# Performance work log

Hardware: AMD Instinct MI355X
Metric: run time of the kernel (lower is better)

## Reference

```python
import jax, jax.numpy as jnp
import numpy as np

DIM = 1024
D_STATE = 64
D_CONV = 4
EXPAND = 2
HEADDIM = 64
D_INNER = EXPAND * DIM                      # 2048
NHEADS = D_INNER // HEADDIM                 # 32
D_CONV_DIM = D_INNER + 2 * D_STATE          # 2176 (ngroups=1)
D_IN_PROJ = 2 * D_INNER + 2 * D_STATE + NHEADS  # 4256


def setup_inputs() -> dict:
    key = jax.random.key(0)
    ks = jax.random.split(key, 9)
    B, L = 4, 2048
    x = jax.random.normal(ks[0], (B, L, DIM), dtype=jnp.float32)
    in_proj_w = jax.random.normal(ks[1], (D_IN_PROJ, DIM), dtype=jnp.float32) * 0.02
    conv_w = jax.random.normal(ks[2], (D_CONV_DIM, D_CONV), dtype=jnp.float32) * 0.2
    conv_b = jax.random.normal(ks[3], (D_CONV_DIM,), dtype=jnp.float32) * 0.02
    # dt bias from inverse-softplus of dt ~ U(1e-3, 0.1) (mamba2 init)
    dt = jnp.exp(jax.random.uniform(ks[4], (NHEADS,)) * (np.log(0.1) - np.log(1e-3)) + np.log(1e-3))
    dt_bias = (dt + jnp.log(-jnp.expm1(-dt))).astype(jnp.float32)
    A_log = jnp.log(jax.random.uniform(ks[5], (NHEADS,), minval=1.0, maxval=16.0)).astype(jnp.float32)
    D = jnp.ones((NHEADS,), dtype=jnp.float32)
    norm_w = jnp.ones((D_INNER,), dtype=jnp.float32)
    out_proj_w = jax.random.normal(ks[6], (DIM, D_INNER), dtype=jnp.float32) * 0.02
    return {"x": x, "in_proj_w": in_proj_w, "conv_w": conv_w, "conv_b": conv_b,
            "dt_bias": dt_bias, "A_log": A_log, "D": D, "norm_w": norm_w,
            "out_proj_w": out_proj_w}


def _mamba2_fwd(x, in_proj_w, conv_w, conv_b, dt_bias, A_log, D, norm_w, out_proj_w):
    B, L, _ = x.shape
    zxbcdt = jnp.einsum('bld,ed->ble', x, in_proj_w)  # (B,L,4256)
    z = zxbcdt[..., :D_INNER]
    xBC = zxbcdt[..., D_INNER:D_INNER + D_CONV_DIM]
    dt = jax.nn.softplus(zxbcdt[..., D_INNER + D_CONV_DIM:] + dt_bias)  # (B,L,H)
    # causal depthwise conv (kernel D_CONV) + silu
    xp = jnp.pad(xBC, ((0, 0), (D_CONV - 1, 0), (0, 0)))
    conv = conv_b
    for k in range(D_CONV):
        conv = conv + xp[:, k:k + L, :] * conv_w[:, k]
    xBC = jax.nn.silu(conv)
    x_ssm = xBC[..., :D_INNER].reshape(B, L, NHEADS, HEADDIM)
    Bm = xBC[..., D_INNER:D_INNER + D_STATE]          # (B,L,N) ngroups=1
    Cm = xBC[..., D_INNER + D_STATE:]                 # (B,L,N)
    A = -jnp.exp(A_log)                               # (H,)

    def step(h, inp):
        xt, Bt, Ct, dtt = inp                         # (B,H,P),(B,N),(B,N),(B,H)
        dA = jnp.exp(dtt * A)                         # (B,H)
        h = h * dA[:, :, None, None] + (dtt[:, :, None] * xt)[..., None] * Bt[:, None, None, :]
        y = jnp.einsum('bhpn,bn->bhp', h, Ct)
        return h, y

    h0 = jnp.zeros((B, NHEADS, HEADDIM, D_STATE), dtype=x.dtype)
    xs = (jnp.swapaxes(x_ssm, 0, 1), jnp.swapaxes(Bm, 0, 1),
          jnp.swapaxes(Cm, 0, 1), jnp.swapaxes(dt, 0, 1))
    _, ys = jax.lax.scan(step, h0, xs)                # (L,B,H,P)
    y = jnp.swapaxes(ys, 0, 1) + x_ssm * D[None, None, :, None]
    y = y.reshape(B, L, D_INNER)
    # gated RMSNorm (norm_before_gate=False): norm(y * silu(z))
    g = y * jax.nn.silu(z)
    g = g * jax.lax.rsqrt(jnp.mean(g * g, axis=-1, keepdims=True) + 1e-5) * norm_w
    return jnp.einsum('ble,de->bld', g, out_proj_w)


def reference(x, in_proj_w, conv_w, conv_b, dt_bias, A_log, D, norm_w, out_proj_w):
    return _mamba2_fwd(x, in_proj_w, conv_w, conv_b, dt_bias, A_log, D, norm_w, out_proj_w)
```

## Files before the change

kernel.cpp:

```cpp
#include <hip/hip_runtime.h>
#include <stdint.h>

typedef unsigned short ushort_t;
typedef __attribute__((ext_vector_type(4))) float f32x4;
typedef __attribute__((ext_vector_type(8))) short short8;
typedef __attribute__((ext_vector_type(4))) unsigned short us4;

#define L_SEQ   2048
#define NROWS   8192
#define KDIM    1024
#define DINNER  2048
#define NHEADS  32
#define DSTATE  64
#define DCONVD  2176
#define NPROJ   4256
#define NPROJP  4352
#define LDZX    4352
#define NCHUNK  32

__device__ __forceinline__ float bf2f(ushort_t u) {
    union { uint32_t i; float f; } v; v.i = ((uint32_t)u) << 16; return v.f;
}
__device__ __forceinline__ ushort_t f2bf(float f) {
    uint32_t x = __float_as_uint(f);
    x += 0x7FFFu + ((x >> 16) & 1u);
    return (ushort_t)(x >> 16);
}
__device__ __forceinline__ int swzi(int row, int col) {
    return row * 64 + (col ^ ((row & 7) << 3));
}

__global__ __launch_bounds__(256) void cast_bf16_kernel(const float* __restrict__ in,
                                                        ushort_t* __restrict__ out, int n4) {
    int i = blockIdx.x * 256 + threadIdx.x;
    if (i >= n4) return;
    float4 v = ((const float4*)in)[i];
    ushort4 o;
    o.x = f2bf(v.x); o.y = f2bf(v.y); o.z = f2bf(v.z); o.w = f2bf(v.w);
    ((ushort4*)out)[i] = o;
}

__global__ __launch_bounds__(256) void cast_pad_w_kernel(const float* __restrict__ w,
                                                         ushort_t* __restrict__ out) {
    int i = blockIdx.x * 256 + threadIdx.x;
    int idx = i * 4;
    int row = idx >> 10;
    ushort4 o;
    if (row < NPROJ) {
        float4 v = ((const float4*)w)[i];
        o.x = f2bf(v.x); o.y = f2bf(v.y); o.z = f2bf(v.z); o.w = f2bf(v.w);
    } else {
        o.x = 0; o.y = 0; o.z = 0; o.w = 0;
    }
    ((ushort4*)out)[i] = o;
}

__device__ __forceinline__ void async16(const void* g, void* l) {
    __builtin_amdgcn_global_load_lds((const __attribute__((address_space(1))) void*)g,
                                     (__attribute__((address_space(3))) void*)l, 16, 0, 0);
}

template<int BN, bool OUT_BF16>
__global__ __launch_bounds__(512, 1) void gemm256_kernel(const ushort_t* __restrict__ Ap,
                                                         const ushort_t* __restrict__ Bp,
                                                         void* __restrict__ Cp,
                                                         const int K, const int ldc,
                                                         const int ntn) {
    constexpr int NBH = BN / 128;
    constexpr int FC  = BN / 64;
    __shared__ ushort_t ldsA[2][2][8192];
    __shared__ ushort_t ldsB[2][NBH][8192];

    const int tid = threadIdx.x;
    const int w = tid >> 6, l = tid & 63;
    const int lr = l & 15, lk = l >> 4;
    const int wm = w >> 2, wn = w & 3;

    const int lin = blockIdx.x;
    const int cpx = gridDim.x >> 3;
    const int swz = (lin & 7) * cpx + (lin >> 3);
    const int nt = swz % ntn, mt = swz / ntn;
    const int m0 = mt * 256, n0 = nt * BN;

    const int row0 = tid >> 3,          c0 = (tid & 7) ^ (row0 & 7);
    const int row1 = (512 + tid) >> 3,  c1 = ((512 + tid) & 7) ^ (row1 & 7);

    const int bcol = wn * (BN / 4);
    const int bh = bcol >> 7, bw0 = bcol & 127;

    f32x4 acc[8][FC];
    const f32x4 zero = {0.f, 0.f, 0.f, 0.f};
#pragma unroll
    for (int i = 0; i < 8; ++i)
#pragma unroll
        for (int j = 0; j < FC; ++j) acc[i][j] = zero;

    auto stage = [&](int d_, int isB, int h_, int ktn) {
        const ushort_t* gb = (isB ? Bp + (size_t)(n0 + h_ * 128) * K
                                  : Ap + (size_t)(m0 + h_ * 128) * K) + (size_t)ktn * 64;
        ushort_t* lb = isB ? &ldsB[d_][h_][0] : &ldsA[d_][h_][0];
        async16(gb + (size_t)row0 * K + c0 * 8, lb + w * 512);
        async16(gb + (size_t)row1 * K + c1 * 8, lb + 4096 + w * 512);
    };

#define COMPUTE_KS(ks_) do {                                                          \
        short8 af[8], bfv[FC];                                                        \
        _Pragma("unroll")                                                             \
        for (int fr = 0; fr < 8; ++fr) {                                              \
            const int ar = fr * 16 + lr;                                              \
            af[fr] = *(const short8*)&Ah[ar * 64 + ((((ks_) * 4 + lk) ^ (ar & 7)) << 3)]; \
        }                                                                             \
        _Pragma("unroll")                                                             \
        for (int fc = 0; fc < FC; ++fc) {                                             \
            const int br = bw0 + fc * 16 + lr;                                        \
            bfv[fc] = *(const short8*)&Bh[br * 64 + ((((ks_) * 4 + lk) ^ (br & 7)) << 3)]; \
        }                                                                             \
        __builtin_amdgcn_s_setprio(1);                                                \
        _Pragma("unroll")                                                             \
        for (int fr = 0; fr < 8; ++fr)                                                \
            _Pragma("unroll")                                                         \
            for (int fc = 0; fc < FC; ++fc)                                           \
                acc[fr][fc] = __builtin_amdgcn_mfma_f32_16x16x32_bf16(                \
                    af[fr], bfv[fc], acc[fr][fc], 0, 0, 0);                           \
        __builtin_amdgcn_s_setprio(0);                                                \
    } while (0)

    stage(0, 0, 0, 0); stage(0, 1, 0, 0);
    stage(0, 0, 1, 0);
    if (NBH == 2) stage(0, 1, 1, 0);

    const int NKT = K >> 6;
    for (int kt = 0; kt < NKT; ++kt) {
        const int d = kt & 1;
        const bool more = (kt + 1 < NKT);
        const ushort_t* Ah = &ldsA[d][wm][0];
        const ushort_t* Bh = &ldsB[d][bh][0];

        if (more) { stage(d ^ 1, 0, 0, kt + 1); stage(d ^ 1, 1, 0, kt + 1); }
        if (more) asm volatile("s_waitcnt vmcnt(4)" ::: "memory");
        else      asm volatile("s_waitcnt vmcnt(0)" ::: "memory");
        __builtin_amdgcn_s_barrier();

        COMPUTE_KS(0);

        if (more) { stage(d ^ 1, 0, 1, kt + 1); if (NBH == 2) stage(d ^ 1, 1, 1, kt + 1); }

        COMPUTE_KS(1);

        __builtin_amdgcn_s_barrier();
    }
#undef COMPUTE_KS

#pragma unroll
    for (int fr2 = 0; fr2 < 8; ++fr2)
#pragma unroll
        for (int fc2 = 0; fc2 < FC; ++fc2) {
            const int col = n0 + bcol + fc2 * 16 + lr;
            const int rowb = m0 + wm * 128 + fr2 * 16 + lk * 4;
#pragma unroll
            for (int r = 0; r < 4; ++r) {
                if (OUT_BF16)
                    ((ushort_t*)Cp)[(size_t)(rowb + r) * ldc + col] = f2bf(acc[fr2][fc2][r]);
                else
                    ((float*)Cp)[(size_t)(rowb + r) * ldc + col] = acc[fr2][fc2][r];
            }
        }
}

__global__ __launch_bounds__(256) void conv_silu_kernel(const ushort_t* __restrict__ zx,
                                                        const float* __restrict__ conv_w,
                                                        const float* __restrict__ conv_b,
                                                        ushort_t* __restrict__ convout) {
    const int idx = blockIdx.x * 256 + threadIdx.x;
    const int row = idx / 272;
    const int c = (idx - row * 272) * 8;
    const int l = row & (L_SEQ - 1);
    float acc[8];
    {
        const float4* bp = (const float4*)(conv_b + c);
        float4 b0 = bp[0], b1 = bp[1];
        acc[0] = b0.x; acc[1] = b0.y; acc[2] = b0.z; acc[3] = b0.w;
        acc[4] = b1.x; acc[5] = b1.y; acc[6] = b1.z; acc[7] = b1.w;
    }
    float wv[8][4];
    {
        const float4* wp = (const float4*)(conv_w + c * 4);
#pragma unroll
        for (int i = 0; i < 8; ++i) {
            float4 t = wp[i];
            wv[i][0] = t.x; wv[i][1] = t.y; wv[i][2] = t.z; wv[i][3] = t.w;
        }
    }
#pragma unroll
    for (int k = 0; k < 4; ++k) {
        const int ll = l - 3 + k;
        if (ll >= 0) {
            short8 v = *(const short8*)(zx + (size_t)(row - 3 + k) * LDZX + DINNER + c);
#pragma unroll
            for (int i = 0; i < 8; ++i)
                acc[i] += bf2f((ushort_t)v[i]) * wv[i][k];
        }
    }
    short8 o;
#pragma unroll
    for (int i = 0; i < 8; ++i) {
        float s = acc[i] / (1.f + expf(-acc[i]));
        o[i] = (short)f2bf(s);
    }
    *(short8*)(convout + (size_t)row * DCONVD + c) = o;
}

__global__ __launch_bounds__(256) void dt_kernel(const ushort_t* __restrict__ zx,
                                                 const float* __restrict__ dt_bias,
                                                 float* __restrict__ dtb) {
    int idx = blockIdx.x * 256 + threadIdx.x;
    int row = idx >> 5;
    int h = idx & 31;
    float v = bf2f(zx[(size_t)row * LDZX + NPROJ - NHEADS + h]) + dt_bias[h];
    dtb[idx] = (v > 20.f) ? v : log1pf(expf(v));
}

__global__ __launch_bounds__(256) void chunk_intra_kernel(
    const ushort_t* __restrict__ cvb, const float* __restrict__ dtb,
    const float* __restrict__ A_log, const float* __restrict__ Dvec,
    ushort_t* __restrict__ ybuf, ushort_t* __restrict__ Gbuf,
    float* __restrict__ expPb)
{
    const int c = blockIdx.x, h = blockIdx.y, b = blockIdx.z;
    const int tid = threadIdx.x;
    const int wv = tid >> 6, lane = tid & 63;
    const int lr = lane & 15, lk = lane >> 4;

    __shared__ __align__(16) ushort_t Cs[4096];
    __shared__ __align__(16) ushort_t Bs[4096];
    __shared__ __align__(16) ushort_t Xt[4096];
    __shared__ __align__(16) ushort_t Ss[4096];
    __shared__ __align__(16) ushort_t Bw[4096];
    __shared__ float sP[64], sdt[64], sWf[64];

    const int t4 = tid >> 2, qq = tid & 3;
    const size_t rowg0 = (size_t)b * L_SEQ + c * 64;
    const ushort_t* rowp = cvb + (rowg0 + t4) * DCONVD;

    short8 rb0 = *(const short8*)(rowp + DINNER + qq * 16);
    short8 rb1 = *(const short8*)(rowp + DINNER + qq * 16 + 8);
    short8 rc0 = *(const short8*)(rowp + DINNER + DSTATE + qq * 16);
    short8 rc1 = *(const short8*)(rowp + DINNER + DSTATE + qq * 16 + 8);
    short8 rx0 = *(const short8*)(rowp + h * 64 + qq * 16);
    short8 rx1 = *(const short8*)(rowp + h * 64 + qq * 16 + 8);

    *(short8*)&Cs[swzi(t4, qq * 16)]     = rc0;
    *(short8*)&Cs[swzi(t4, qq * 16 + 8)] = rc1;
    *(short8*)&Bs[swzi(t4, qq * 16)]     = rb0;
    *(short8*)&Bs[swzi(t4, qq * 16 + 8)] = rb1;
#pragma unroll
    for (int k = 0; k < 8; ++k) {
        Xt[swzi(qq * 16 + k, t4)]     = (ushort_t)rx0[k];
        Xt[swzi(qq * 16 + 8 + k, t4)] = (ushort_t)rx1[k];
    }
    if (tid < 64) {
        float dt = dtb[(rowg0 + tid) * NHEADS + h];
        float A = -__expf(A_log[h]);
        float P = dt * A;
#pragma unroll
        for (int off = 1; off < 64; off <<= 1) {
            float o = __shfl_up(P, off);
            if (tid >= off) P += o;
        }
        sP[tid] = P;
        sdt[tid] = dt;
        float P63 = __shfl(P, 63);
        sWf[tid] = __expf(P63 - P) * dt;
        expPb[(size_t)(b * NHEADS + h) * L_SEQ + c * 64 + tid] = __expf(P);
    }
    __syncthreads();

    {
        const float w = sWf[t4];
#pragma unroll
        for (int k = 0; k < 8; ++k) {
            Bw[swzi(qq * 16 + k, t4)]     = f2bf(bf2f((ushort_t)rb0[k]) * w);
            Bw[swzi(qq * 16 + 8 + k, t4)] = f2bf(bf2f((ushort_t)rb1[k]) * w);
        }
    }

    const float Dh = Dvec[h];
    {
        short8 a0 = *(const short8*)&Cs[swzi(wv * 16 + lr, lk * 8)];
        short8 a1 = *(const short8*)&Cs[swzi(wv * 16 + lr, 32 + lk * 8)];
        f32x4 acc[4];
        const f32x4 zero = {0.f, 0.f, 0.f, 0.f};
#pragma unroll
        for (int nj = 0; nj < 4; ++nj) {
            short8 b0 = *(const short8*)&Bs[swzi(nj * 16 + lr, lk * 8)];
            short8 b1 = *(const short8*)&Bs[swzi(nj * 16 + lr, 32 + lk * 8)];
            acc[nj] = __builtin_amdgcn_mfma_f32_16x16x32_bf16(a0, b0, zero, 0, 0, 0);
            acc[nj] = __builtin_amdgcn_mfma_f32_16x16x32_bf16(a1, b1, acc[nj], 0, 0, 0);
        }
#pragma unroll
        for (int r = 0; r < 4; ++r) {
            const int i = wv * 16 + lk * 4 + r;
            const float Pi = sP[i];
#pragma unroll
            for (int nj = 0; nj < 4; ++nj) {
                const int j = nj * 16 + lr;
                float s = 0.f;
                if (j <= i) s = acc[nj][r] * __expf(Pi - sP[j]) * sdt[j];
                if (j == i) s += Dh;
                Ss[swzi(i, j)] = f2bf(s);
            }
        }
    }
    __syncthreads();

    {
        short8 a0 = *(const short8*)&Ss[swzi(wv * 16 + lr, lk * 8)];
        short8 a1 = *(const short8*)&Ss[swzi(wv * 16 + lr, 32 + lk * 8)];
        const f32x4 zero = {0.f, 0.f, 0.f, 0.f};
#pragma unroll
        for (int np = 0; np < 4; ++np) {
            short8 b0 = *(const short8*)&Xt[swzi(np * 16 + lr, lk * 8)];
            short8 b1 = *(const short8*)&Xt[swzi(np * 16 + lr, 32 + lk * 8)];
            f32x4 acc = __builtin_amdgcn_mfma_f32_16x16x32_bf16(a0, b0, zero, 0, 0, 0);
            acc = __builtin_amdgcn_mfma_f32_16x16x32_bf16(a1, b1, acc, 0, 0, 0);
#pragma unroll
            for (int r = 0; r < 4; ++r) {
                const int i = wv * 16 + lk * 4 + r;
                const int p = np * 16 + lr;
                ybuf[(rowg0 + i) * DINNER + (size_t)h * 64 + p] = f2bf(acc[r]);
            }
        }
    }

    {
        short8 a0 = *(const short8*)&Xt[swzi(wv * 16 + lr, lk * 8)];
        short8 a1 = *(const short8*)&Xt[swzi(wv * 16 + lr, 32 + lk * 8)];
        const f32x4 zero = {0.f, 0.f, 0.f, 0.f};
        const size_t gbase = ((size_t)((b * NHEADS + h) * NCHUNK + c)) << 12;
#pragma unroll
        for (int nt = 0; nt < 4; ++nt) {
            short8 b0 = *(const short8*)&Bw[swzi(nt * 16 + lr, lk * 8)];
            short8 b1 = *(const short8*)&Bw[swzi(nt * 16 + lr, 32 + lk * 8)];
            f32x4 acc = __builtin_amdgcn_mfma_f32_16x16x32_bf16(a0, b0, zero, 0, 0, 0);
            acc = __builtin_amdgcn_mfma_f32_16x16x32_bf16(a1, b1, acc, 0, 0, 0);
#pragma unroll
            for (int r = 0; r < 4; ++r) {
                const int p = wv * 16 + lk * 4 + r;
                const int n = nt * 16 + lr;
                Gbuf[gbase + p * 64 + n] = f2bf(acc[r]);
            }
        }
    }
}

__global__ __launch_bounds__(256) void state_scan_kernel(
    ushort_t* __restrict__ GH, const float* __restrict__ expPb)
{
    const int half = blockIdx.x, h = blockIdx.y, b = blockIdx.z;
    const int bh = b * NHEADS + h;
    const int e0 = half * 2048 + threadIdx.x * 8;
    ushort_t* base = GH + ((size_t)bh << 17);
    const float* ep = expPb + (size_t)bh * L_SEQ;

    float hr[8];
#pragma unroll
    for (int k = 0; k < 8; ++k) hr[k] = 0.f;

    short8 g = *(const short8*)(base + e0);
    float Ec = ep[63];
    for (int c = 0; c < NCHUNK; ++c) {
        short8 gn = g; float En = 0.f;
        if (c + 1 < NCHUNK) {
            gn = *(const short8*)(base + ((size_t)(c + 1) << 12) + e0);
            En = ep[(c + 1) * 64 + 63];
        }
        short8 o;
#pragma unroll
        for (int k = 0; k < 8; ++k) o[k] = (short)f2bf(hr[k]);
        *(short8*)(base + ((size_t)c << 12) + e0) = o;
#pragma unroll
        for (int k = 0; k < 8; ++k) hr[k] = hr[k] * Ec + bf2f((ushort_t)g[k]);
        g = gn; Ec = En;
    }
}

__global__ __launch_bounds__(256) void y_inter_kernel(
    const ushort_t* __restrict__ cvb, const float* __restrict__ expPb,
    const ushort_t* __restrict__ hst, ushort_t* __restrict__ ybuf)
{
    const int c = blockIdx.x + 1, h = blockIdx.y, b = blockIdx.z;
    const int tid = threadIdx.x;
    const int wv = tid >> 6, lane = tid & 63;
    const int lr = lane & 15, lk = lane >> 4;
    const int bh = b * NHEADS + h;

    __shared__ __align__(16) ushort_t Cs[4096];
    __shared__ __align__(16) ushort_t Hp[4096];
    __shared__ float sEp[64];

    const int t4 = tid >> 2, qq = tid & 3;
    const size_t rowg0 = (size_t)b * L_SEQ + c * 64;
    {
        const ushort_t* rp = cvb + (rowg0 + t4) * DCONVD + DINNER + DSTATE + qq * 16;
        *(short8*)&Cs[swzi(t4, qq * 16)]     = *(const short8*)rp;
        *(short8*)&Cs[swzi(t4, qq * 16 + 8)] = *(const short8*)(rp + 8);
        const ushort_t* hr = hst + (((size_t)(bh * NCHUNK + c)) << 12) + t4 * 64 + qq * 16;
        *(short8*)&Hp[swzi(t4, qq * 16)]     = *(const short8*)hr;
        *(short8*)&Hp[swzi(t4, qq * 16 + 8)] = *(const short8*)(hr + 8);
    }
    if (tid < 64) sEp[tid] = expPb[(size_t)bh * L_SEQ + c * 64 + tid];
    __syncthreads();

    short8 a0 = *(const short8*)&Cs[swzi(wv * 16 + lr, lk * 8)];
    short8 a1 = *(const short8*)&Cs[swzi(wv * 16 + lr, 32 + lk * 8)];
    const f32x4 zero = {0.f, 0.f, 0.f, 0.f};
#pragma unroll
    for (int np = 0; np < 4; ++np) {
        short8 b0 = *(const short8*)&Hp[swzi(np * 16 + lr, lk * 8)];
        short8 b1 = *(const short8*)&Hp[swzi(np * 16 + lr, 32 + lk * 8)];
        f32x4 acc = __builtin_amdgcn_mfma_f32_16x16x32_bf16(a0, b0, zero, 0, 0, 0);
        acc = __builtin_amdgcn_mfma_f32_16x16x32_bf16(a1, b1, acc, 0, 0, 0);
#pragma unroll
        for (int r = 0; r < 4; ++r) {
            const int t = wv * 16 + lk * 4 + r;
            const int p = np * 16 + lr;
            ushort_t* yp = &ybuf[(rowg0 + t) * DINNER + (size_t)h * 64 + p];
            *yp = f2bf(bf2f(*yp) + acc[r] * sEp[t]);
        }
    }
}

__global__ __launch_bounds__(256) void gatenorm_kernel(const ushort_t* __restrict__ ybuf,
                                                       const ushort_t* __restrict__ zx,
                                                       const float* __restrict__ norm_w,
                                                       ushort_t* __restrict__ gbuf) {
    const int row = blockIdx.x;
    const int tid = threadIdx.x;
    short8 yv = *(const short8*)(ybuf + (size_t)row * DINNER + tid * 8);
    short8 zv = *(const short8*)(zx + (size_t)row * LDZX + tid * 8);
    float g[8];
    float ss = 0.f;
#pragma unroll
    for (int i = 0; i < 8; ++i) {
        float y = bf2f((ushort_t)yv[i]);
        float z = bf2f((ushort_t)zv[i]);
        float sz = z / (1.f + expf(-z));
        float gg = y * sz;
        g[i] = gg;
        ss += gg * gg;
    }
#pragma unroll
    for (int o = 32; o > 0; o >>= 1) ss += __shfl_xor(ss, o);
    __shared__ float wsum[4];
    if ((tid & 63) == 0) wsum[tid >> 6] = ss;
    __syncthreads();
    float tot = wsum[0] + wsum[1] + wsum[2] + wsum[3];
    float scale = rsqrtf(tot * (1.0f / (float)DINNER) + 1e-5f);
    short8 o8;
#pragma unroll
    for (int i = 0; i < 8; ++i)
        o8[i] = (short)f2bf(g[i] * scale * norm_w[tid * 8 + i]);
    *(short8*)(gbuf + (size_t)row * DINNER + tid * 8) = o8;
}

extern "C" void kernel_launch(void* const* d_in, const int* in_sizes, int n_in,
                              void* d_out, int out_size, void* d_ws, size_t ws_size,
                              hipStream_t stream) {
    const float* x          = (const float*)d_in[0];
    const float* in_proj_w  = (const float*)d_in[1];
    const float* conv_w     = (const float*)d_in[2];
    const float* conv_b     = (const float*)d_in[3];
    const float* dt_bias    = (const float*)d_in[4];
    const float* A_log      = (const float*)d_in[5];
    const float* Dvec       = (const float*)d_in[6];
    const float* norm_w     = (const float*)d_in[7];
    const float* out_proj_w = (const float*)d_in[8];
    float* out = (float*)d_out;

    char* ws = (char*)d_ws;
    size_t off = 0;
    ushort_t* owbf  = (ushort_t*)(ws + off); off += (size_t)KDIM * DINNER * 2;
    ushort_t* zx    = (ushort_t*)(ws + off); off += (size_t)NROWS * LDZX * 2;
    ushort_t* cvb   = (ushort_t*)(ws + off); off += (size_t)NROWS * DCONVD * 2;
    float*    dtb   = (float*)(ws + off);    off += (size_t)NROWS * NHEADS * 4;
    float*    expPb = (float*)(ws + off);    off += (size_t)128 * L_SEQ * 4;
    ushort_t* ybuf  = (ushort_t*)(ws + off); off += (size_t)NROWS * DINNER * 2;
    char* tail = ws + off;
    ushort_t* xbf  = (ushort_t*)tail;
    ushort_t* wbf  = (ushort_t*)(tail + (size_t)NROWS * KDIM * 2);
    ushort_t* Gbuf = (ushort_t*)tail;
    ushort_t* gbuf = (ushort_t*)tail;

    cast_bf16_kernel<<<8192, 256, 0, stream>>>(x, xbf, NROWS * KDIM / 4);
    cast_pad_w_kernel<<<4352, 256, 0, stream>>>(in_proj_w, wbf);
    cast_bf16_kernel<<<2048, 256, 0, stream>>>(out_proj_w, owbf, KDIM * DINNER / 4);

    gemm256_kernel<256, true><<<544, 512, 0, stream>>>(xbf, wbf, zx, KDIM, LDZX, 17);

    conv_silu_kernel<<<NROWS * 272 / 256, 256, 0, stream>>>(zx, conv_w, conv_b, cvb);

    dt_kernel<<<NROWS * NHEADS / 256, 256, 0, stream>>>(zx, dt_bias, dtb);

    chunk_intra_kernel<<<dim3(NCHUNK, NHEADS, 4), 256, 0, stream>>>(
        cvb, dtb, A_log, Dvec, ybuf, Gbuf, expPb);
    state_scan_kernel<<<dim3(2, NHEADS, 4), 256, 0, stream>>>(Gbuf, expPb);
    y_inter_kernel<<<dim3(NCHUNK - 1, NHEADS, 4), 256, 0, stream>>>(
        cvb, expPb, Gbuf, ybuf);

    gatenorm_kernel<<<NROWS, 256, 0, stream>>>(ybuf, zx, norm_w, gbuf);

    gemm256_kernel<128, false><<<256, 512, 0, stream>>>(gbuf, owbf, out, DINNER, KDIM, 8);
}
```

Measured before the change: 329.2 us.

## Restructure GEMM main loop into four-phase k-half pipeline and fuse dt softplus

```diff
diff --git a/kernel.cpp b/kernel.cpp
--- a/kernel.cpp
+++ b/kernel.cpp
@@ -66,10 +66,11 @@
                                                          void* __restrict__ Cp,
                                                          const int K, const int ldc,
                                                          const int ntn) {
-    constexpr int NBH = BN / 128;
-    constexpr int FC  = BN / 64;
-    __shared__ ushort_t ldsA[2][2][8192];
-    __shared__ ushort_t ldsB[2][NBH][8192];
+    constexpr int FC = BN / 64;
+    constexpr int LB = BN / 128;
+    constexpr int VN = 2 + LB;
+    __shared__ ushort_t ldsA[2][2][256 * 32];
+    __shared__ ushort_t ldsB[2][2][BN * 32];
 
     const int tid = threadIdx.x;
     const int w = tid >> 6, l = tid & 63;
@@ -81,12 +82,10 @@
     const int swz = (lin & 7) * cpx + (lin >> 3);
     const int nt = swz % ntn, mt = swz / ntn;
     const int m0 = mt * 256, n0 = nt * BN;
-
-    const int row0 = tid >> 3,          c0 = (tid & 7) ^ (row0 & 7);
-    const int row1 = (512 + tid) >> 3,  c1 = ((512 + tid) & 7) ^ (row1 & 7);
-
     const int bcol = wn * (BN / 4);
-    const int bh = bcol >> 7, bw0 = bcol & 127;
+
+    const int sr0 = tid >> 2,         sg0 = (tid & 3) ^ (sr0 & 3) ^ ((sr0 >> 2) & 3);
+    const int sr1 = (512 + tid) >> 2, sg1 = ((512 + tid) & 3) ^ (sr1 & 3) ^ ((sr1 >> 2) & 3);
 
     f32x4 acc[8][FC];
     const f32x4 zero = {0.f, 0.f, 0.f, 0.f};
@@ -95,61 +94,73 @@
 #pragma unroll
         for (int j = 0; j < FC; ++j) acc[i][j] = zero;
 
-    auto stage = [&](int d_, int isB, int h_, int ktn) {
-        const ushort_t* gb = (isB ? Bp + (size_t)(n0 + h_ * 128) * K
-                                  : Ap + (size_t)(m0 + h_ * 128) * K) + (size_t)ktn * 64;
-        ushort_t* lb = isB ? &ldsB[d_][h_][0] : &ldsA[d_][h_][0];
-        async16(gb + (size_t)row0 * K + c0 * 8, lb + w * 512);
-        async16(gb + (size_t)row1 * K + c1 * 8, lb + 4096 + w * 512);
+    auto stageA = [&](int d_, int kh, int ktn) {
+        const ushort_t* gb = Ap + (size_t)m0 * K + (size_t)ktn * 64 + kh * 32;
+        async16(gb + (size_t)sr0 * K + sg0 * 8, (ushort_t*)&ldsA[d_][kh][0] + tid * 8);
+        async16(gb + (size_t)sr1 * K + sg1 * 8, (ushort_t*)&ldsA[d_][kh][0] + (512 + tid) * 8);
     };
-
-#define COMPUTE_KS(ks_) do {                                                          \
-        short8 af[8], bfv[FC];                                                        \
-        _Pragma("unroll")                                                             \
-        for (int fr = 0; fr < 8; ++fr) {                                              \
-            const int ar = fr * 16 + lr;                                              \
-            af[fr] = *(const short8*)&Ah[ar * 64 + ((((ks_) * 4 + lk) ^ (ar & 7)) << 3)]; \
-        }                                                                             \
-        _Pragma("unroll")                                                             \
-        for (int fc = 0; fc < FC; ++fc) {                                             \
-            const int br = bw0 + fc * 16 + lr;                                        \
-            bfv[fc] = *(const short8*)&Bh[br * 64 + ((((ks_) * 4 + lk) ^ (br & 7)) << 3)]; \
-        }                                                                             \
-        __builtin_amdgcn_s_setprio(1);                                                \
-        _Pragma("unroll")                                                             \
-        for (int fr = 0; fr < 8; ++fr)                                                \
-            _Pragma("unroll")                                                         \
-            for (int fc = 0; fc < FC; ++fc)                                           \
-                acc[fr][fc] = __builtin_amdgcn_mfma_f32_16x16x32_bf16(                \
-                    af[fr], bfv[fc], acc[fr][fc], 0, 0, 0);                           \
-        __builtin_amdgcn_s_setprio(0);                                                \
+    auto stageB = [&](int d_, int kh, int ktn) {
+        const ushort_t* gb = Bp + (size_t)n0 * K + (size_t)ktn * 64 + kh * 32;
+        async16(gb + (size_t)sr0 * K + sg0 * 8, (ushort_t*)&ldsB[d_][kh][0] + tid * 8);
+        if constexpr (LB == 2)
+            async16(gb + (size_t)sr1 * K + sg1 * 8, (ushort_t*)&ldsB[d_][kh][0] + (512 + tid) * 8);
+    };
+
+#define VMWAIT_VN do { if constexpr (VN == 4) asm volatile("s_waitcnt vmcnt(4)" ::: "memory"); \
+                       else                   asm volatile("s_waitcnt vmcnt(3)" ::: "memory"); } while (0)
+#define VMWAIT_0  asm volatile("s_waitcnt vmcnt(0)" ::: "memory")
+
+    short8 bfv[FC];
+
+#define PHASE(ks_, frh_, STAGE_STMT, VM_STMT) do {                                      \
+        short8 af[4];                                                                   \
+        _Pragma("unroll")                                                               \
+        for (int fr = 0; fr < 4; ++fr) {                                                \
+            const int row = wm * 128 + ((frh_) * 4 + fr) * 16 + lr;                     \
+            const int sl = lk ^ (row & 3) ^ ((row >> 2) & 3);                           \
+            af[fr] = *(const short8*)&ldsA[d][ks_][row * 32 + sl * 8];                  \
+        }                                                                               \
+        if ((frh_) == 0) {                                                              \
+            _Pragma("unroll")                                                           \
+            for (int fc = 0; fc < FC; ++fc) {                                           \
+                const int row = bcol + fc * 16 + lr;                                    \
+                const int sl = lk ^ (row & 3) ^ ((row >> 2) & 3);                       \
+                bfv[fc] = *(const short8*)&ldsB[d][ks_][row * 32 + sl * 8];             \
+            }                                                                           \
+        }                                                                               \
+        STAGE_STMT;                                                                     \
+        __builtin_amdgcn_s_barrier();                                                   \
+        __builtin_amdgcn_s_setprio(1);                                                  \
+        _Pragma("unroll")                                                               \
+        for (int fr = 0; fr < 4; ++fr)                                                  \
+            _Pragma("unroll")                                                           \
+            for (int fc = 0; fc < FC; ++fc)                                             \
+                acc[(frh_) * 4 + fr][fc] = __builtin_amdgcn_mfma_f32_16x16x32_bf16(     \
+                    af[fr], bfv[fc], acc[(frh_) * 4 + fr][fc], 0, 0, 0);                \
+        __builtin_amdgcn_s_setprio(0);                                                  \
+        VM_STMT;                                                                        \
+        __builtin_amdgcn_s_barrier();                                                   \
     } while (0)
 
-    stage(0, 0, 0, 0); stage(0, 1, 0, 0);
-    stage(0, 0, 1, 0);
-    if (NBH == 2) stage(0, 1, 1, 0);
+    stageA(0, 0, 0); stageB(0, 0, 0);
+    stageA(0, 1, 0); stageB(0, 1, 0);
+    VMWAIT_VN;
+    __builtin_amdgcn_s_barrier();
 
     const int NKT = K >> 6;
     for (int kt = 0; kt < NKT; ++kt) {
         const int d = kt & 1;
         const bool more = (kt + 1 < NKT);
-        const ushort_t* Ah = &ldsA[d][wm][0];
-        const ushort_t* Bh = &ldsB[d][bh][0];
-
-        if (more) { stage(d ^ 1, 0, 0, kt + 1); stage(d ^ 1, 1, 0, kt + 1); }
-        if (more) asm volatile("s_waitcnt vmcnt(4)" ::: "memory");
-        else      asm volatile("s_waitcnt vmcnt(0)" ::: "memory");
-        __builtin_amdgcn_s_barrier();
-
-        COMPUTE_KS(0);
-
-        if (more) { stage(d ^ 1, 0, 1, kt + 1); if (NBH == 2) stage(d ^ 1, 1, 1, kt + 1); }
-
-        COMPUTE_KS(1);
-
-        __builtin_amdgcn_s_barrier();
-    }
-#undef COMPUTE_KS
+        PHASE(0, 0, { if (more) stageA(d ^ 1, 0, kt + 1); }, {});
+        PHASE(0, 1, { if (more) stageB(d ^ 1, 0, kt + 1); },
+                    { if (more) VMWAIT_VN; else VMWAIT_0; });
+        PHASE(1, 0, { if (more) stageA(d ^ 1, 1, kt + 1); }, {});
+        PHASE(1, 1, { if (more) stageB(d ^ 1, 1, kt + 1); },
+                    { if (more) VMWAIT_VN; });
+    }
+#undef PHASE
+#undef VMWAIT_VN
+#undef VMWAIT_0
 
 #pragma unroll
     for (int fr2 = 0; fr2 < 8; ++fr2)
@@ -210,18 +221,9 @@
     *(short8*)(convout + (size_t)row * DCONVD + c) = o;
 }
 
-__global__ __launch_bounds__(256) void dt_kernel(const ushort_t* __restrict__ zx,
-                                                 const float* __restrict__ dt_bias,
-                                                 float* __restrict__ dtb) {
-    int idx = blockIdx.x * 256 + threadIdx.x;
-    int row = idx >> 5;
-    int h = idx & 31;
-    float v = bf2f(zx[(size_t)row * LDZX + NPROJ - NHEADS + h]) + dt_bias[h];
-    dtb[idx] = (v > 20.f) ? v : log1pf(expf(v));
-}
-
 __global__ __launch_bounds__(256) void chunk_intra_kernel(
-    const ushort_t* __restrict__ cvb, const float* __restrict__ dtb,
+    const ushort_t* __restrict__ cvb, const ushort_t* __restrict__ zx,
+    const float* __restrict__ dt_bias,
     const float* __restrict__ A_log, const float* __restrict__ Dvec,
     ushort_t* __restrict__ ybuf, ushort_t* __restrict__ Gbuf,
     float* __restrict__ expPb)
@@ -259,7 +261,8 @@
         Xt[swzi(qq * 16 + 8 + k, t4)] = (ushort_t)rx1[k];
     }
     if (tid < 64) {
-        float dt = dtb[(rowg0 + tid) * NHEADS + h];
+        float dv = bf2f(zx[(rowg0 + tid) * LDZX + (NPROJ - NHEADS) + h]) + dt_bias[h];
+        float dt = (dv > 20.f) ? dv : log1pf(expf(dv));
         float A = -__expf(A_log[h]);
         float P = dt * A;
 #pragma unroll
@@ -482,7 +485,6 @@
     ushort_t* owbf  = (ushort_t*)(ws + off); off += (size_t)KDIM * DINNER * 2;
     ushort_t* zx    = (ushort_t*)(ws + off); off += (size_t)NROWS * LDZX * 2;
     ushort_t* cvb   = (ushort_t*)(ws + off); off += (size_t)NROWS * DCONVD * 2;
-    float*    dtb   = (float*)(ws + off);    off += (size_t)NROWS * NHEADS * 4;
     float*    expPb = (float*)(ws + off);    off += (size_t)128 * L_SEQ * 4;
     ushort_t* ybuf  = (ushort_t*)(ws + off); off += (size_t)NROWS * DINNER * 2;
     char* tail = ws + off;
@@ -499,10 +501,8 @@
 
     conv_silu_kernel<<<NROWS * 272 / 256, 256, 0, stream>>>(zx, conv_w, conv_b, cvb);
 
-    dt_kernel<<<NROWS * NHEADS / 256, 256, 0, stream>>>(zx, dt_bias, dtb);
-
     chunk_intra_kernel<<<dim3(NCHUNK, NHEADS, 4), 256, 0, stream>>>(
-        cvb, dtb, A_log, Dvec, ybuf, Gbuf, expPb);
+        cvb, zx, dt_bias, A_log, Dvec, ybuf, Gbuf, expPb);
     state_scan_kernel<<<dim3(2, NHEADS, 4), 256, 0, stream>>>(Gbuf, expPb);
     y_inter_kernel<<<dim3(NCHUNK - 1, NHEADS, 4), 256, 0, stream>>>(
         cvb, expPb, Gbuf, ybuf);
```

Result: no change. 325.7 us (-1.1%).

## Fuse conv+silu and softplus dt into chunk kernel, use 128-tile in_proj GEMM

Applied to the files above, without the earlier changes.

```diff
diff --git a/kernel.cpp b/kernel.cpp
--- a/kernel.cpp
+++ b/kernel.cpp
@@ -58,6 +58,102 @@
 __device__ __forceinline__ void async16(const void* g, void* l) {
     __builtin_amdgcn_global_load_lds((const __attribute__((address_space(1))) void*)g,
                                      (__attribute__((address_space(3))) void*)l, 16, 0, 0);
+}
+
+__global__ __launch_bounds__(256, 2) void gemm128_kernel(const ushort_t* __restrict__ Ap,
+                                                         const ushort_t* __restrict__ Bp,
+                                                         ushort_t* __restrict__ Cx) {
+    __shared__ ushort_t ldsA[2][8192];
+    __shared__ ushort_t ldsB[2][8192];
+    const int tid = threadIdx.x;
+    const int w = tid >> 6, l = tid & 63;
+    const int lr = l & 15, lk = l >> 4;
+    const int wm = w >> 1, wn = w & 1;
+
+    const int lin = blockIdx.x;
+    const int swz = (lin & 7) * 272 + (lin >> 3);
+    const int nt = swz % 34, mt = swz / 34;
+    const int m0 = mt * 128, n0 = nt * 128;
+
+    int srow[4], scol[4];
+#pragma unroll
+    for (int i = 0; i < 4; ++i) {
+        int s = i * 256 + tid;
+        srow[i] = s >> 3;
+        scol[i] = (s & 7) ^ (srow[i] & 7);
+    }
+
+    f32x4 acc[4][4];
+    const f32x4 zero = {0.f, 0.f, 0.f, 0.f};
+#pragma unroll
+    for (int i = 0; i < 4; ++i)
+#pragma unroll
+        for (int j = 0; j < 4; ++j) acc[i][j] = zero;
+
+    auto stageA = [&](int d_, int ktn) {
+        const ushort_t* gb = Ap + (size_t)m0 * KDIM + (size_t)ktn * 64;
+#pragma unroll
+        for (int i = 0; i < 4; ++i)
+            async16(gb + (size_t)srow[i] * KDIM + scol[i] * 8, &ldsA[d_][(i * 256 + tid) * 8]);
+    };
+    auto stageB = [&](int d_, int ktn) {
+        const ushort_t* gb = Bp + (size_t)n0 * KDIM + (size_t)ktn * 64;
+#pragma unroll
+        for (int i = 0; i < 4; ++i)
+            async16(gb + (size_t)srow[i] * KDIM + scol[i] * 8, &ldsB[d_][(i * 256 + tid) * 8]);
+    };
+
+#define CKS(ks_) do {                                                                   \
+        short8 af[4], bfv[4];                                                           \
+        _Pragma("unroll")                                                               \
+        for (int fr = 0; fr < 4; ++fr) {                                                \
+            const int ar = wm * 64 + fr * 16 + lr;                                      \
+            af[fr] = *(const short8*)&ldsA[d][ar * 64 + ((((ks_) * 4 + lk) ^ (ar & 7)) << 3)]; \
+        }                                                                               \
+        _Pragma("unroll")                                                               \
+        for (int fc = 0; fc < 4; ++fc) {                                                \
+            const int br = wn * 64 + fc * 16 + lr;                                      \
+            bfv[fc] = *(const short8*)&ldsB[d][br * 64 + ((((ks_) * 4 + lk) ^ (br & 7)) << 3)]; \
+        }                                                                               \
+        __builtin_amdgcn_s_setprio(1);                                                  \
+        _Pragma("unroll")                                                               \
+        for (int fr = 0; fr < 4; ++fr)                                                  \
+            _Pragma("unroll")                                                           \
+            for (int fc = 0; fc < 4; ++fc)                                              \
+                acc[fr][fc] = __builtin_amdgcn_mfma_f32_16x16x32_bf16(                  \
+                    af[fr], bfv[fc], acc[fr][fc], 0, 0, 0);                             \
+        __builtin_amdgcn_s_setprio(0);                                                  \
+    } while (0)
+
+    stageA(0, 0); stageB(0, 0);
+    asm volatile("s_waitcnt vmcnt(0)" ::: "memory");
+    __builtin_amdgcn_s_barrier();
+
+    const int NKT = KDIM >> 6;
+    for (int kt = 0; kt < NKT; ++kt) {
+        const int d = kt & 1;
+        const bool more = (kt + 1 < NKT);
+        if (more) stageA(d ^ 1, kt + 1);
+        if (more) asm volatile("s_waitcnt vmcnt(4)" ::: "memory");
+        else      asm volatile("s_waitcnt vmcnt(0)" ::: "memory");
+        __builtin_amdgcn_s_barrier();
+        CKS(0);
+        if (more) stageB(d ^ 1, kt + 1);
+        CKS(1);
+        __builtin_amdgcn_s_barrier();
+    }
+#undef CKS
+
+#pragma unroll
+    for (int fr2 = 0; fr2 < 4; ++fr2)
+#pragma unroll
+        for (int fc2 = 0; fc2 < 4; ++fc2) {
+            const int col = n0 + wn * 64 + fc2 * 16 + lr;
+            const int rowb = m0 + wm * 64 + fr2 * 16 + lk * 4;
+#pragma unroll
+            for (int r = 0; r < 4; ++r)
+                Cx[(size_t)(rowb + r) * LDZX + col] = f2bf(acc[fr2][fc2][r]);
+        }
 }
 
 template<int BN, bool OUT_BF16>
@@ -167,64 +263,12 @@
         }
 }
 
-__global__ __launch_bounds__(256) void conv_silu_kernel(const ushort_t* __restrict__ zx,
-                                                        const float* __restrict__ conv_w,
-                                                        const float* __restrict__ conv_b,
-                                                        ushort_t* __restrict__ convout) {
-    const int idx = blockIdx.x * 256 + threadIdx.x;
-    const int row = idx / 272;
-    const int c = (idx - row * 272) * 8;
-    const int l = row & (L_SEQ - 1);
-    float acc[8];
-    {
-        const float4* bp = (const float4*)(conv_b + c);
-        float4 b0 = bp[0], b1 = bp[1];
-        acc[0] = b0.x; acc[1] = b0.y; acc[2] = b0.z; acc[3] = b0.w;
-        acc[4] = b1.x; acc[5] = b1.y; acc[6] = b1.z; acc[7] = b1.w;
-    }
-    float wv[8][4];
-    {
-        const float4* wp = (const float4*)(conv_w + c * 4);
-#pragma unroll
-        for (int i = 0; i < 8; ++i) {
-            float4 t = wp[i];
-            wv[i][0] = t.x; wv[i][1] = t.y; wv[i][2] = t.z; wv[i][3] = t.w;
-        }
-    }
-#pragma unroll
-    for (int k = 0; k < 4; ++k) {
-        const int ll = l - 3 + k;
-        if (ll >= 0) {
-            short8 v = *(const short8*)(zx + (size_t)(row - 3 + k) * LDZX + DINNER + c);
-#pragma unroll
-            for (int i = 0; i < 8; ++i)
-                acc[i] += bf2f((ushort_t)v[i]) * wv[i][k];
-        }
-    }
-    short8 o;
-#pragma unroll
-    for (int i = 0; i < 8; ++i) {
-        float s = acc[i] / (1.f + expf(-acc[i]));
-        o[i] = (short)f2bf(s);
-    }
-    *(short8*)(convout + (size_t)row * DCONVD + c) = o;
-}
-
-__global__ __launch_bounds__(256) void dt_kernel(const ushort_t* __restrict__ zx,
-                                                 const float* __restrict__ dt_bias,
-                                                 float* __restrict__ dtb) {
-    int idx = blockIdx.x * 256 + threadIdx.x;
-    int row = idx >> 5;
-    int h = idx & 31;
-    float v = bf2f(zx[(size_t)row * LDZX + NPROJ - NHEADS + h]) + dt_bias[h];
-    dtb[idx] = (v > 20.f) ? v : log1pf(expf(v));
-}
-
 __global__ __launch_bounds__(256) void chunk_intra_kernel(
-    const ushort_t* __restrict__ cvb, const float* __restrict__ dtb,
+    const ushort_t* __restrict__ zx, const float* __restrict__ conv_w,
+    const float* __restrict__ conv_b, const float* __restrict__ dt_bias,
     const float* __restrict__ A_log, const float* __restrict__ Dvec,
     ushort_t* __restrict__ ybuf, ushort_t* __restrict__ Gbuf,
-    float* __restrict__ expPb)
+    float* __restrict__ expPb, ushort_t* __restrict__ Cbuf)
 {
     const int c = blockIdx.x, h = blockIdx.y, b = blockIdx.z;
     const int tid = threadIdx.x;
@@ -239,15 +283,49 @@
     __shared__ float sP[64], sdt[64], sWf[64];
 
     const int t4 = tid >> 2, qq = tid & 3;
+    const int l_ = c * 64 + t4;
     const size_t rowg0 = (size_t)b * L_SEQ + c * 64;
-    const ushort_t* rowp = cvb + (rowg0 + t4) * DCONVD;
-
-    short8 rb0 = *(const short8*)(rowp + DINNER + qq * 16);
-    short8 rb1 = *(const short8*)(rowp + DINNER + qq * 16 + 8);
-    short8 rc0 = *(const short8*)(rowp + DINNER + DSTATE + qq * 16);
-    short8 rc1 = *(const short8*)(rowp + DINNER + DSTATE + qq * 16 + 8);
-    short8 rx0 = *(const short8*)(rowp + h * 64 + qq * 16);
-    short8 rx1 = *(const short8*)(rowp + h * 64 + qq * 16 + 8);
+    const size_t grow = rowg0 + t4;
+
+    auto conv8 = [&](int zc, int wc) -> short8 {
+        float a[8]; float4 wvv[8];
+#pragma unroll
+        for (int j = 0; j < 8; ++j) {
+            a[j] = conv_b[wc + j];
+            wvv[j] = *(const float4*)(conv_w + (wc + j) * 4);
+        }
+#pragma unroll
+        for (int k = 0; k < 4; ++k) {
+            if (l_ - 3 + k >= 0) {
+                short8 v = *(const short8*)(zx + (grow - 3 + k) * LDZX + zc);
+#pragma unroll
+                for (int j = 0; j < 8; ++j) {
+                    float wk = (k == 0) ? wvv[j].x : (k == 1) ? wvv[j].y
+                             : (k == 2) ? wvv[j].z : wvv[j].w;
+                    a[j] += bf2f((ushort_t)v[j]) * wk;
+                }
+            }
+        }
+        short8 o;
+#pragma unroll
+        for (int j = 0; j < 8; ++j) {
+            float s = a[j] / (1.f + expf(-a[j]));
+            o[j] = (short)f2bf(s);
+        }
+        return o;
+    };
+
+    short8 rb0 = conv8(4096 + qq * 16,            2048 + qq * 16);
+    short8 rb1 = conv8(4096 + qq * 16 + 8,        2048 + qq * 16 + 8);
+    short8 rc0 = conv8(4160 + qq * 16,            2112 + qq * 16);
+    short8 rc1 = conv8(4160 + qq * 16 + 8,        2112 + qq * 16 + 8);
+    short8 rx0 = conv8(2048 + h * 64 + qq * 16,      h * 64 + qq * 16);
+    short8 rx1 = conv8(2048 + h * 64 + qq * 16 + 8,  h * 64 + qq * 16 + 8);
+
+    if (h == 0) {
+        *(short8*)(Cbuf + grow * 64 + qq * 16)     = rc0;
+        *(short8*)(Cbuf + grow * 64 + qq * 16 + 8) = rc1;
+    }
 
     *(short8*)&Cs[swzi(t4, qq * 16)]     = rc0;
     *(short8*)&Cs[swzi(t4, qq * 16 + 8)] = rc1;
@@ -259,7 +337,8 @@
         Xt[swzi(qq * 16 + 8 + k, t4)] = (ushort_t)rx1[k];
     }
     if (tid < 64) {
-        float dt = dtb[(rowg0 + tid) * NHEADS + h];
+        float dv = bf2f(zx[(rowg0 + tid) * LDZX + (NPROJ - NHEADS) + h]) + dt_bias[h];
+        float dt = (dv > 20.f) ? dv : log1pf(expf(dv));
         float A = -__expf(A_log[h]);
         float P = dt * A;
 #pragma unroll
@@ -385,7 +464,7 @@
 }
 
 __global__ __launch_bounds__(256) void y_inter_kernel(
-    const ushort_t* __restrict__ cvb, const float* __restrict__ expPb,
+    const ushort_t* __restrict__ Cbuf, const float* __restrict__ expPb,
     const ushort_t* __restrict__ hst, ushort_t* __restrict__ ybuf)
 {
     const int c = blockIdx.x + 1, h = blockIdx.y, b = blockIdx.z;
@@ -401,7 +480,7 @@
     const int t4 = tid >> 2, qq = tid & 3;
     const size_t rowg0 = (size_t)b * L_SEQ + c * 64;
     {
-        const ushort_t* rp = cvb + (rowg0 + t4) * DCONVD + DINNER + DSTATE + qq * 16;
+        const ushort_t* rp = Cbuf + (rowg0 + t4) * 64 + qq * 16;
         *(short8*)&Cs[swzi(t4, qq * 16)]     = *(const short8*)rp;
         *(short8*)&Cs[swzi(t4, qq * 16 + 8)] = *(const short8*)(rp + 8);
         const ushort_t* hr = hst + (((size_t)(bh * NCHUNK + c)) << 12) + t4 * 64 + qq * 16;
@@ -481,8 +560,7 @@
     size_t off = 0;
     ushort_t* owbf  = (ushort_t*)(ws + off); off += (size_t)KDIM * DINNER * 2;
     ushort_t* zx    = (ushort_t*)(ws + off); off += (size_t)NROWS * LDZX * 2;
-    ushort_t* cvb   = (ushort_t*)(ws + off); off += (size_t)NROWS * DCONVD * 2;
-    float*    dtb   = (float*)(ws + off);    off += (size_t)NROWS * NHEADS * 4;
+    ushort_t* Cbuf  = (ushort_t*)(ws + off); off += (size_t)NROWS * 64 * 2;
     float*    expPb = (float*)(ws + off);    off += (size_t)128 * L_SEQ * 4;
     ushort_t* ybuf  = (ushort_t*)(ws + off); off += (size_t)NROWS * DINNER * 2;
     char* tail = ws + off;
@@ -495,17 +573,13 @@
     cast_pad_w_kernel<<<4352, 256, 0, stream>>>(in_proj_w, wbf);
     cast_bf16_kernel<<<2048, 256, 0, stream>>>(out_proj_w, owbf, KDIM * DINNER / 4);
 
-    gemm256_kernel<256, true><<<544, 512, 0, stream>>>(xbf, wbf, zx, KDIM, LDZX, 17);
-
-    conv_silu_kernel<<<NROWS * 272 / 256, 256, 0, stream>>>(zx, conv_w, conv_b, cvb);
-
-    dt_kernel<<<NROWS * NHEADS / 256, 256, 0, stream>>>(zx, dt_bias, dtb);
+    gemm128_kernel<<<2176, 256, 0, stream>>>(xbf, wbf, zx);
 
     chunk_intra_kernel<<<dim3(NCHUNK, NHEADS, 4), 256, 0, stream>>>(
-        cvb, dtb, A_log, Dvec, ybuf, Gbuf, expPb);
+        zx, conv_w, conv_b, dt_bias, A_log, Dvec, ybuf, Gbuf, expPb, Cbuf);
     state_scan_kernel<<<dim3(2, NHEADS, 4), 256, 0, stream>>>(Gbuf, expPb);
     y_inter_kernel<<<dim3(NCHUNK - 1, NHEADS, 4), 256, 0, stream>>>(
-        cvb, expPb, Gbuf, ybuf);
+        Cbuf, expPb, Gbuf, ybuf);
 
     gatenorm_kernel<<<NROWS, 256, 0, stream>>>(ybuf, zx, norm_w, gbuf);
 
```

New measurement: 392.9 us. +19.3%, slower.
